# Kernel optimization log

Measured on AMD Instinct MI355X. Metric: run time of the kernel, lower is better.

The kernel has to match this reference:

```python
import jax, jax.numpy as jnp
import numpy as np

N_NODES = 100000
N_EDGES = 1000000
N_GRAPHS = 64
IN_F, H_F, N_CLS = 64, 64, 16
N_RELS = 8
N_BASES = 8  # DGL default: num_bases = num_rels when None


def setup_inputs() -> dict:
    key = jax.random.key(0)
    ks = jax.random.split(key, 16)
    in_feat = jax.random.normal(ks[0], (N_NODES, IN_F), dtype=jnp.float32)
    src = jax.random.randint(ks[1], (N_EDGES,), 0, N_NODES)
    dst = jax.random.randint(ks[2], (N_EDGES,), 0, N_NODES)
    etypes = jax.random.randint(ks[3], (N_EDGES,), 0, N_RELS)
    graph_ids = jnp.sort(jax.random.randint(ks[4], (N_NODES,), 0, N_GRAPHS))
    s1 = 1.0 / np.sqrt(IN_F)
    s2 = 1.0 / np.sqrt(H_F)
    bases1 = jax.random.normal(ks[5], (N_BASES, IN_F, H_F), dtype=jnp.float32) * s1
    coeff1 = jax.random.normal(ks[6], (N_RELS, N_BASES), dtype=jnp.float32) * (1.0 / np.sqrt(N_BASES))
    wself1 = jax.random.normal(ks[7], (IN_F, H_F), dtype=jnp.float32) * s1
    bias1 = jnp.zeros((H_F,), dtype=jnp.float32)
    bases2 = jax.random.normal(ks[8], (N_BASES, H_F, N_CLS), dtype=jnp.float32) * s2
    coeff2 = jax.random.normal(ks[9], (N_RELS, N_BASES), dtype=jnp.float32) * (1.0 / np.sqrt(N_BASES))
    wself2 = jax.random.normal(ks[10], (H_F, N_CLS), dtype=jnp.float32) * s2
    bias2 = jnp.zeros((N_CLS,), dtype=jnp.float32)
    return {"in_feat": in_feat, "src": src, "dst": dst, "etypes": etypes,
            "graph_ids": graph_ids, "bases1": bases1, "coeff1": coeff1,
            "wself1": wself1, "bias1": bias1, "bases2": bases2,
            "coeff2": coeff2, "wself2": wself2, "bias2": bias2}


def _rel_graph_conv(x, src, dst, etypes, bases, coeff, wself, bias):
    # Basis decomposition: W_r = sum_b coeff[r,b] * bases[b]
    W = jnp.einsum('rb,bio->rio', coeff, bases)          # [R, in, out]
    # Project every node under every relation (R small), then gather per edge.
    xw = jnp.einsum('ni,rio->rno', x, W)                 # [R, N, out]
    msg = xw[etypes, src]                                 # [E, out]
    agg = jax.ops.segment_sum(msg, dst, num_segments=x.shape[0])
    # DGL defaults: self_loop=True, bias=True
    return agg + x @ wself + bias


def reference(in_feat, src, dst, etypes, graph_ids,
              bases1, coeff1, wself1, bias1,
              bases2, coeff2, wself2, bias2):
    h = _rel_graph_conv(in_feat, src, dst, etypes, bases1, coeff1, wself1, bias1)
    h = jax.nn.relu(h)
    h = _rel_graph_conv(h, src, dst, etypes, bases2, coeff2, wself2, bias2)
    h = jax.nn.relu(h)
    # dgl.mean_nodes: per-graph mean over node features
    sums = jax.ops.segment_sum(h, graph_ids, num_segments=N_GRAPHS)   # [G, C]
    counts = jax.ops.segment_sum(jnp.ones((h.shape[0],), h.dtype), graph_ids,
                                 num_segments=N_GRAPHS)
    return sums / jnp.maximum(counts, 1.0)[:, None]
```

## Files before the change

### kernel.cpp

```cpp
#include <hip/hip_runtime.h>


typedef __attribute__((ext_vector_type(8))) short bf16x8;
typedef __attribute__((ext_vector_type(4))) float f32x4;

#define NBLK 256

__device__ __forceinline__ unsigned short f2bf(float f) {
    unsigned u = __float_as_uint(f);
    unsigned r = u + 0x7FFFu + ((u >> 16) & 1u);
    return (unsigned short)(r >> 16);
}

__device__ __forceinline__ float bf2f(unsigned short u) {
    return __uint_as_float(((unsigned)u) << 16);
}

__device__ __forceinline__ unsigned pk2(float lo, float hi) {
    unsigned r;
    asm("v_cvt_pk_bf16_f32 %0, %1, %2" : "=v"(r) : "v"(lo), "v"(hi));
    return r;
}

union cv16 { uint4 u; bf16x8 b; };

__device__ __forceinline__ void acc8(uint4 m, float* a) {
    a[0] += bf2f((unsigned short)m.x); a[1] += bf2f((unsigned short)(m.x >> 16));
    a[2] += bf2f((unsigned short)m.y); a[3] += bf2f((unsigned short)(m.y >> 16));
    a[4] += bf2f((unsigned short)m.z); a[5] += bf2f((unsigned short)(m.z >> 16));
    a[6] += bf2f((unsigned short)m.w); a[7] += bf2f((unsigned short)(m.w >> 16));
}

__global__ __launch_bounds__(256) void k_bhist_w(
    const int* __restrict__ dst, int* __restrict__ bh, int nE, int nBins,
    const float* __restrict__ bases1, const float* __restrict__ coeff1,
    const float* __restrict__ bases2, const float* __restrict__ coeff2,
    const float* __restrict__ wself1, const float* __restrict__ wself2,
    unsigned short* __restrict__ W1f, unsigned short* __restrict__ W2f,
    unsigned short* __restrict__ W1sf, unsigned short* __restrict__ W2sf) {
    if (blockIdx.x >= NBLK) {
        int r = blockIdx.x - NBLK;
        int tid = threadIdx.x;
        float c1[8], c2[8];
#pragma unroll
        for (int b = 0; b < 8; ++b) { c1[b] = coeff1[r * 8 + b]; c2[b] = coeff2[r * 8 + b]; }
        for (int idx = tid; idx < 4096; idx += 256) {
            int j = idx & 7, lane = (idx >> 3) & 63, nt = (idx >> 9) & 3, kt = idx >> 11;
            int i = kt * 32 + ((lane >> 4) << 3) + j;
            int jo = nt * 16 + (lane & 15);
            float s = 0.f;
#pragma unroll
            for (int b = 0; b < 8; ++b) s = fmaf(c1[b], bases1[b * 4096 + i * 64 + jo], s);
            W1f[r * 4096 + idx] = f2bf(s);
            if (r == 0) W1sf[idx] = f2bf(wself1[i * 64 + jo]);
        }
        for (int idx = tid; idx < 1024; idx += 256) {
            int j = idx & 7, lane = (idx >> 3) & 63, kt = idx >> 9;
            int i = kt * 32 + ((lane >> 4) << 3) + j;
            int jo = lane & 15;
            float s = 0.f;
#pragma unroll
            for (int b = 0; b < 8; ++b) s = fmaf(c2[b], bases2[b * 1024 + i * 16 + jo], s);
            W2f[r * 1024 + idx] = f2bf(s);
            if (r == 0) W2sf[idx] = f2bf(wself2[i * 16 + jo]);
        }
        return;
    }
    __shared__ int h[512];
    for (int i = threadIdx.x; i < 512; i += 256) h[i] = 0;
    __syncthreads();
    int blk = blockIdx.x;
    int ech = (nE + NBLK - 1) / NBLK;
    int e0 = blk * ech, e1 = min(e0 + ech, nE);
    for (int e = e0 + threadIdx.x; e < e1; e += 256)
        atomicAdd(&h[dst[e] >> 8], 1);
    __syncthreads();
    for (int t = threadIdx.x; t < nBins; t += 256) bh[t * NBLK + blk] = h[t];
}

__global__ __launch_bounds__(256) void k_scanblk(
    const int* __restrict__ in, int* __restrict__ outx,
    int* __restrict__ btot, int n) {
    __shared__ int sm[256];
    int tid = threadIdx.x;
    int i = blockIdx.x * 256 + tid;
    int d = (i < n) ? in[i] : 0;
    sm[tid] = d;
    __syncthreads();
#pragma unroll
    for (int off = 1; off < 256; off <<= 1) {
        int v = (tid >= off) ? sm[tid - off] : 0;
        __syncthreads();
        sm[tid] += v;
        __syncthreads();
    }
    if (i < n) outx[i] = sm[tid] - d;
    if (tid == 255) btot[blockIdx.x] = sm[255];
}

__global__ void k_scantop(const int* __restrict__ btot, int* __restrict__ boff, int nB) {
    __shared__ int sm[512];
    int t = threadIdx.x;
    int d = (t < nB) ? btot[t] : 0;
    sm[t] = d;
    __syncthreads();
#pragma unroll
    for (int off = 1; off < 512; off <<= 1) {
        int v = (t >= off) ? sm[t - off] : 0;
        __syncthreads();
        sm[t] += v;
        __syncthreads();
    }
    if (t < nB) boff[t] = sm[t] - d;
}

#define XW1S 44
__global__ __launch_bounds__(256) void k_mega(
    const int* __restrict__ dst, const int* __restrict__ src,
    const int* __restrict__ et, const int* __restrict__ bhs,
    const int* __restrict__ boff, int* __restrict__ payload,
    int nE, int nBins,
    const float* __restrict__ x,
    const unsigned short* __restrict__ W1f,
    const unsigned short* __restrict__ W1sf,
    const float* __restrict__ bias1,
    unsigned short* __restrict__ xw1, int nNodes) {
    __shared__ int cur[512];
    __shared__ unsigned lds[4][16 * XW1S];
    if (blockIdx.x < NBLK) {
        int blk = blockIdx.x;
        for (int t = threadIdx.x; t < nBins; t += 256)
            cur[t] = bhs[t * NBLK + blk] + boff[t];
        __syncthreads();
        int ech = (nE + NBLK - 1) / NBLK;
        int e0 = blk * ech, e1 = min(e0 + ech, nE);
        for (int e = e0 + threadIdx.x; e < e1; e += 256) {
            int d = dst[e];
            int pos = atomicAdd(&cur[d >> 8], 1);
            payload[pos] = ((src[e] * 9 + et[e]) << 8) | (d & 255);
        }
        return;
    }
    int lane = threadIdx.x & 63;
    int wid = (int)(threadIdx.x >> 6);
    int tile = (blockIdx.x - NBLK) * 4 + wid;
    int n0 = tile * 16;
    if (n0 >= nNodes) return;
    int sA = n0 + (lane & 15);
    if (sA >= nNodes) sA = nNodes - 1;
    const float* xrow = x + (size_t)sA * 64 + ((lane >> 4) << 3);
    bf16x8 a[2];
#pragma unroll
    for (int kt = 0; kt < 2; ++kt) {
        f32x4 u0 = *(const f32x4*)(xrow + kt * 32);
        f32x4 u1 = *(const f32x4*)(xrow + kt * 32 + 4);
        cv16 c;
        c.u.x = pk2(u0[0], u0[1]);
        c.u.y = pk2(u0[2], u0[3]);
        c.u.z = pk2(u1[0], u1[1]);
        c.u.w = pk2(u1[2], u1[3]);
        a[kt] = c.b;
    }
    float bj[4];
#pragma unroll
    for (int nt = 0; nt < 4; ++nt) bj[nt] = bias1[nt * 16 + (lane & 15)];
    unsigned* L = lds[wid];
    const int even = !(lane & 1);
    const int cpair = (lane & 14) >> 1;
    int row2 = lane >> 2, ch = lane & 3;
    int nOut = n0 + row2;
    for (int r = 0; r < 9; ++r) {
        const unsigned short* Wf = (r < 8) ? (W1f + r * 4096) : W1sf;
        f32x4 z = {0.f, 0.f, 0.f, 0.f};
        f32x4 acc[4] = {z, z, z, z};
#pragma unroll
        for (int kt = 0; kt < 2; ++kt)
#pragma unroll
            for (int nt = 0; nt < 4; ++nt) {
                bf16x8 b = *(const bf16x8*)(Wf + (kt * 4 + nt) * 512 + lane * 8);
                acc[nt] = __builtin_amdgcn_mfma_f32_16x16x32_bf16(a[kt], b, acc[nt], 0, 0, 0);
            }
        if (r == 8) {
#pragma unroll
            for (int nt = 0; nt < 4; ++nt)
#pragma unroll
                for (int reg = 0; reg < 4; ++reg) acc[nt][reg] += bj[nt];
        }
#pragma unroll
        for (int reg = 0; reg < 4; ++reg) {
            int row = ((lane >> 4) << 2) + reg;
#pragma unroll
            for (int nt = 0; nt < 4; ++nt) {
                float mine = acc[nt][reg];
                float oth = __shfl_xor(mine, 1, 64);
                unsigned pk = even ? pk2(mine, oth) : pk2(oth, mine);
                if (even ? (nt < 2) : (nt >= 2)) L[row * XW1S + cpair + nt * 8] = pk;
            }
        }
        if (nOut < nNodes) {
            uint4 v0 = *(uint4*)&L[row2 * XW1S + ch * 4];
            uint4 v1 = *(uint4*)&L[row2 * XW1S + 16 + ch * 4];
            uint4* mp = (uint4*)(xw1 + ((size_t)nOut * 9 + r) * 64);
            mp[ch] = v0;
            mp[4 + ch] = v1;
        }
    }
}

__global__ __launch_bounds__(256) void k_brefine(
    const int* __restrict__ payload, const int* __restrict__ bhs,
    const int* __restrict__ boff,
    int* __restrict__ skey, int* __restrict__ nodeoff,
    int nE, int nBins, int nNodes) {
    __shared__ int h[256];
    __shared__ int cur[256];
    __shared__ int sm[256];
    int b = blockIdx.x;
    int e0 = bhs[b * NBLK] + boff[b];
    int e1 = (b + 1 < nBins) ? (bhs[(b + 1) * NBLK] + boff[b + 1]) : nE;
    int t = threadIdx.x;
    h[t] = 0;
    __syncthreads();
    for (int e = e0 + t; e < e1; e += 256)
        atomicAdd(&h[payload[e] & 255], 1);
    __syncthreads();
    int d = h[t];
    sm[t] = d;
    __syncthreads();
#pragma unroll
    for (int off = 1; off < 256; off <<= 1) {
        int v = (t >= off) ? sm[t - off] : 0;
        __syncthreads();
        sm[t] += v;
        __syncthreads();
    }
    int excl = sm[t] - d;
    cur[t] = excl;
    int n = (b << 8) + t;
    if (n < nNodes) nodeoff[n] = e0 + excl;
    __syncthreads();
    for (int e = e0 + t; e < e1; e += 256) {
        int pay = payload[e];
        int pos = atomicAdd(&cur[pay & 255], 1);
        skey[e0 + pos] = pay >> 8;
    }
    if (b == 0 && t == 0) nodeoff[nNodes] = nE;
}

__global__ __launch_bounds__(256) void k_f1(
    const unsigned short* __restrict__ xw1, const int* __restrict__ skey,
    const int* __restrict__ nodeoff,
    const unsigned short* __restrict__ W2f,
    const unsigned short* __restrict__ W2sf,
    const float* __restrict__ bias2,
    unsigned short* __restrict__ xw2, int nNodes) {
    __shared__ uint4 hbuf[64][9];
    __shared__ unsigned tlds[4][16 * 12];
    int t = threadIdx.x;
    int n0blk = blockIdx.x * 64;
    int gl = t & 7;
    int grp = t >> 3;
    for (int pass = 0; pass < 2; ++pass) {
        int nn = pass * 32 + grp;
        int n = n0blk + nn;
        uint4 p = {0, 0, 0, 0};
        if (n < nNodes) {
            int s0 = nodeoff[n], s1 = nodeoff[n + 1];
            uint4 v = *(const uint4*)(xw1 + ((size_t)n * 9 + 8) * 64 + gl * 8);
            float a[8];
            a[0] = bf2f((unsigned short)v.x); a[1] = bf2f((unsigned short)(v.x >> 16));
            a[2] = bf2f((unsigned short)v.y); a[3] = bf2f((unsigned short)(v.y >> 16));
            a[4] = bf2f((unsigned short)v.z); a[5] = bf2f((unsigned short)(v.z >> 16));
            a[6] = bf2f((unsigned short)v.w); a[7] = bf2f((unsigned short)(v.w >> 16));
            int i = s0;
            for (; i + 4 <= s1; i += 4) {
                int k0 = skey[i], k1 = skey[i + 1], k2 = skey[i + 2], k3 = skey[i + 3];
                uint4 m0 = *(const uint4*)(xw1 + (size_t)k0 * 64 + gl * 8);
                uint4 m1 = *(const uint4*)(xw1 + (size_t)k1 * 64 + gl * 8);
                uint4 m2 = *(const uint4*)(xw1 + (size_t)k2 * 64 + gl * 8);
                uint4 m3 = *(const uint4*)(xw1 + (size_t)k3 * 64 + gl * 8);
                acc8(m0, a); acc8(m1, a); acc8(m2, a); acc8(m3, a);
            }
            for (; i < s1; ++i) {
                uint4 m = *(const uint4*)(xw1 + (size_t)skey[i] * 64 + gl * 8);
                acc8(m, a);
            }
#pragma unroll
            for (int q = 0; q < 8; ++q) a[q] = fmaxf(a[q], 0.f);
            p.x = pk2(a[0], a[1]);
            p.y = pk2(a[2], a[3]);
            p.z = pk2(a[4], a[5]);
            p.w = pk2(a[6], a[7]);
        }
        hbuf[nn][gl] = p;
    }
    __syncthreads();
    int lane = t & 63;
    int w = t >> 6;
    int arow = w * 16 + (lane & 15);
    cv16 c0, c1;
    c0.u = hbuf[arow][lane >> 4];
    c1.u = hbuf[arow][4 + (lane >> 4)];
    bf16x8 a0 = c0.b, a1 = c1.b;
    float bj = bias2[lane & 15];
    unsigned* L = tlds[w];
    const int even = !(lane & 1);
    const int cpair = (lane & 14) >> 1;
    int row2 = lane >> 1, ch = lane & 1;
    int nOut = n0blk + w * 16 + row2;
    for (int r = 0; r < 9; ++r) {
        const unsigned short* Wf = (r < 8) ? (W2f + r * 1024) : W2sf;
        bf16x8 b0 = *(const bf16x8*)(Wf + lane * 8);
        bf16x8 b1 = *(const bf16x8*)(Wf + 512 + lane * 8);
        f32x4 acc = {0.f, 0.f, 0.f, 0.f};
        acc = __builtin_amdgcn_mfma_f32_16x16x32_bf16(a0, b0, acc, 0, 0, 0);
        acc = __builtin_amdgcn_mfma_f32_16x16x32_bf16(a1, b1, acc, 0, 0, 0);
        if (r == 8) {
#pragma unroll
            for (int reg = 0; reg < 4; ++reg) acc[reg] += bj;
        }
#pragma unroll
        for (int reg = 0; reg < 4; ++reg) {
            int row = ((lane >> 4) << 2) + reg;
            float mine = acc[reg];
            float oth = __shfl_xor(mine, 1, 64);
            unsigned pk = even ? pk2(mine, oth) : pk2(oth, mine);
            if (even ? (reg < 2) : (reg >= 2)) L[row * 12 + cpair] = pk;
        }
        if (lane < 32 && nOut < nNodes) {
            uint4 v = *(uint4*)&L[row2 * 12 + ch * 4];
            ((uint4*)(xw2 + ((size_t)nOut * 9 + r) * 16))[ch] = v;
        }
    }
}

__global__ __launch_bounds__(256) void k_seg2f(
    unsigned short* __restrict__ xw2, const int* __restrict__ skey,
    const int* __restrict__ nodeoff, int nNodes) {
    int gl = threadIdx.x & 1;
    int grp = (int)((blockIdx.x * blockDim.x + threadIdx.x) >> 1);
    int nG = (int)((gridDim.x * blockDim.x) >> 1);
    for (int n = grp; n < nNodes; n += nG) {
        int s0 = nodeoff[n], s1 = nodeoff[n + 1];
        uint4 v = *(const uint4*)(xw2 + ((size_t)n * 9 + 8) * 16 + gl * 8);
        float a[8];
        a[0] = bf2f((unsigned short)v.x); a[1] = bf2f((unsigned short)(v.x >> 16));
        a[2] = bf2f((unsigned short)v.y); a[3] = bf2f((unsigned short)(v.y >> 16));
        a[4] = bf2f((unsigned short)v.z); a[5] = bf2f((unsigned short)(v.z >> 16));
        a[6] = bf2f((unsigned short)v.w); a[7] = bf2f((unsigned short)(v.w >> 16));
        int i = s0;
        for (; i + 4 <= s1; i += 4) {
            int k0 = skey[i], k1 = skey[i + 1], k2 = skey[i + 2], k3 = skey[i + 3];
            uint4 m0 = *(const uint4*)(xw2 + (size_t)k0 * 16 + gl * 8);
            uint4 m1 = *(const uint4*)(xw2 + (size_t)k1 * 16 + gl * 8);
            uint4 m2 = *(const uint4*)(xw2 + (size_t)k2 * 16 + gl * 8);
            uint4 m3 = *(const uint4*)(xw2 + (size_t)k3 * 16 + gl * 8);
            acc8(m0, a); acc8(m1, a); acc8(m2, a); acc8(m3, a);
        }
        for (; i < s1; ++i) {
            uint4 m = *(const uint4*)(xw2 + (size_t)skey[i] * 16 + gl * 8);
            acc8(m, a);
        }
        uint4 p;
        p.x = pk2(a[0], a[1]);
        p.y = pk2(a[2], a[3]);
        p.z = pk2(a[4], a[5]);
        p.w = pk2(a[6], a[7]);
        *(uint4*)(xw2 + ((size_t)n * 9 + 8) * 16 + gl * 8) = p;
    }
}

__global__ __launch_bounds__(256) void k_pool(
    const unsigned short* __restrict__ xw2, const int* __restrict__ gid,
    float* __restrict__ out, int nNodes) {
    __shared__ float sm[256];
    __shared__ int bnd[2];
    int g = blockIdx.x;
    int t = threadIdx.x;
    if (t < 2) {
        int target = g + t;
        int lo = 0, hi = nNodes;
        while (lo < hi) {
            int mid = (lo + hi) >> 1;
            if (gid[mid] < target) lo = mid + 1; else hi = mid;
        }
        bnd[t] = lo;
    }
    __syncthreads();
    int s0 = bnd[0], s1 = bnd[1];
    int c = t & 15, idx = t >> 4;
    float acc = 0.f;
    for (int n = s0 + idx; n < s1; n += 16)
        acc += fmaxf(bf2f(xw2[((size_t)n * 9 + 8) * 16 + c]), 0.f);
    sm[t] = acc;
    __syncthreads();
#pragma unroll
    for (int off = 128; off >= 16; off >>= 1) {
        if (t < off) sm[t] += sm[t + off];
        __syncthreads();
    }
    if (t < 16) {
        float cnt = (float)(s1 - s0);
        out[g * 16 + t] = sm[t] / fmaxf(cnt, 1.f);
    }
}

extern "C" void kernel_launch(void* const* d_in, const int* in_sizes, int n_in,
                              void* d_out, int out_size, void* d_ws, size_t ws_size,
                              hipStream_t stream) {
    const float* x      = (const float*)d_in[0];
    const int*   src    = (const int*)d_in[1];
    const int*   dst    = (const int*)d_in[2];
    const int*   et     = (const int*)d_in[3];
    const int*   gid    = (const int*)d_in[4];
    const float* bases1 = (const float*)d_in[5];
    const float* coeff1 = (const float*)d_in[6];
    const float* wself1 = (const float*)d_in[7];
    const float* bias1  = (const float*)d_in[8];
    const float* bases2 = (const float*)d_in[9];
    const float* coeff2 = (const float*)d_in[10];
    const float* wself2 = (const float*)d_in[11];
    const float* bias2  = (const float*)d_in[12];
    float* out = (float*)d_out;

    int nNodes = in_sizes[0] / 64;
    int nE = in_sizes[1];
    int nBins = (nNodes + 255) >> 8;
    int nBh = nBins * NBLK;

    char* ws = (char*)d_ws;
    unsigned short* W1f  = (unsigned short*)(ws);
    unsigned short* W2f  = (unsigned short*)(ws + 65536);
    unsigned short* W1sf = (unsigned short*)(ws + 81920);
    unsigned short* W2sf = (unsigned short*)(ws + 90112);
    int*   payload = (int*)(ws + 92160);
    int*   skey    = (int*)(ws + 4092160);
    int*   nodeoff = (int*)(ws + 8092160);
    int*   bh      = (int*)(ws + 8492288);
    int*   bhs     = (int*)(ws + 8892672);
    int*   btot    = (int*)(ws + 9293056);
    int*   boff    = (int*)(ws + 9295104);
    unsigned short* xw1 = (unsigned short*)(ws + 9297152);
    unsigned short* xw2 = (unsigned short*)(ws + 124497152);

    int tiles = (nNodes + 15) / 16;
    int xwb = (tiles + 3) / 4;
    int f1b = (nNodes + 63) / 64;
    int scb = (nBh + 255) / 256;

    hipLaunchKernelGGL(k_bhist_w, dim3(NBLK + 8), dim3(256), 0, stream,
                       dst, bh, nE, nBins,
                       bases1, coeff1, bases2, coeff2, wself1, wself2,
                       W1f, W2f, W1sf, W2sf);
    hipLaunchKernelGGL(k_scanblk, dim3(scb), dim3(256), 0, stream,
                       bh, bhs, btot, nBh);
    hipLaunchKernelGGL(k_scantop, dim3(1), dim3(512), 0, stream, btot, boff, scb);
    hipLaunchKernelGGL(k_mega, dim3(NBLK + xwb), dim3(256), 0, stream,
                       dst, src, et, bhs, boff, payload, nE, nBins,
                       x, W1f, W1sf, bias1, xw1, nNodes);
    hipLaunchKernelGGL(k_brefine, dim3(nBins), dim3(256), 0, stream,
                       payload, bhs, boff, skey, nodeoff, nE, nBins, nNodes);
    hipLaunchKernelGGL(k_f1, dim3(f1b), dim3(256), 0, stream,
                       xw1, skey, nodeoff, W2f, W2sf, bias2, xw2, nNodes);
    hipLaunchKernelGGL(k_seg2f, dim3(1024), dim3(256), 0, stream,
                       xw2, skey, nodeoff, nNodes);
    hipLaunchKernelGGL(k_pool, dim3(64), dim3(256), 0, stream,
                       xw2, gid, out, nNodes);
}
```

Baseline: 167.4 us.

## Split layer-1 projection across scatter and refine kernels to overlap work

The layer-1 node projection (xw1 MFMA tiles) was previously fused only with the edge scatter kernel, and the bucket-refine kernel ran alone with just nBins blocks. Now a single kernel template handles both phases, and each launch computes half of the projection tiles, so the refine phase also has independent GEMM work to fill the GPU. The aim is to hide the low-occupancy refine kernel behind useful compute. In exchange the LDS footprint per block grows and the block-index roles are reordered, with projection blocks first and sort blocks last.

```diff
diff --git a/kernel.cpp b/kernel.cpp
--- a/kernel.cpp
+++ b/kernel.cpp
@@ -5,6 +5,7 @@
 typedef __attribute__((ext_vector_type(4))) float f32x4;
 
 #define NBLK 256
+#define XW1S 44
 
 __device__ __forceinline__ unsigned short f2bf(float f) {
     unsigned u = __float_as_uint(f);
@@ -114,36 +115,71 @@
     if (t < nB) boff[t] = sm[t] - d;
 }
 
-#define XW1S 44
-__global__ __launch_bounds__(256) void k_mega(
+__global__ __launch_bounds__(256) void k_megax(
+    int phase, int tileOff, int xwbThis,
     const int* __restrict__ dst, const int* __restrict__ src,
     const int* __restrict__ et, const int* __restrict__ bhs,
     const int* __restrict__ boff, int* __restrict__ payload,
-    int nE, int nBins,
+    int* __restrict__ skey, int* __restrict__ nodeoff, int nE, int nBins,
     const float* __restrict__ x,
     const unsigned short* __restrict__ W1f,
     const unsigned short* __restrict__ W1sf,
     const float* __restrict__ bias1,
     unsigned short* __restrict__ xw1, int nNodes) {
-    __shared__ int cur[512];
     __shared__ unsigned lds[4][16 * XW1S];
-    if (blockIdx.x < NBLK) {
-        int blk = blockIdx.x;
-        for (int t = threadIdx.x; t < nBins; t += 256)
-            cur[t] = bhs[t * NBLK + blk] + boff[t];
-        __syncthreads();
-        int ech = (nE + NBLK - 1) / NBLK;
-        int e0 = blk * ech, e1 = min(e0 + ech, nE);
-        for (int e = e0 + threadIdx.x; e < e1; e += 256) {
-            int d = dst[e];
-            int pos = atomicAdd(&cur[d >> 8], 1);
-            payload[pos] = ((src[e] * 9 + et[e]) << 8) | (d & 255);
+    __shared__ int scur[512];
+    __shared__ int sh[256];
+    __shared__ int ssm[256];
+    if ((int)blockIdx.x >= xwbThis) {
+        int sb = blockIdx.x - xwbThis;
+        int t = threadIdx.x;
+        if (phase == 0) {
+            for (int q = t; q < nBins; q += 256)
+                scur[q] = bhs[q * NBLK + sb] + boff[q];
+            __syncthreads();
+            int ech = (nE + NBLK - 1) / NBLK;
+            int e0 = sb * ech, e1 = min(e0 + ech, nE);
+            for (int e = e0 + t; e < e1; e += 256) {
+                int d = dst[e];
+                int pos = atomicAdd(&scur[d >> 8], 1);
+                payload[pos] = ((src[e] * 9 + et[e]) << 8) | (d & 255);
+            }
+        } else {
+            int b = sb;
+            int e0 = bhs[b * NBLK] + boff[b];
+            int e1 = (b + 1 < nBins) ? (bhs[(b + 1) * NBLK] + boff[b + 1]) : nE;
+            sh[t] = 0;
+            __syncthreads();
+            for (int e = e0 + t; e < e1; e += 256)
+                atomicAdd(&sh[payload[e] & 255], 1);
+            __syncthreads();
+            int d = sh[t];
+            ssm[t] = d;
+            __syncthreads();
+#pragma unroll
+            for (int off = 1; off < 256; off <<= 1) {
+                int v = (t >= off) ? ssm[t - off] : 0;
+                __syncthreads();
+                ssm[t] += v;
+                __syncthreads();
+            }
+            int excl = ssm[t] - d;
+            scur[t] = excl;
+            int n = (b << 8) + t;
+            if (n < nNodes) nodeoff[n] = e0 + excl;
+            __syncthreads();
+            for (int e = e0 + t; e < e1; e += 256) {
+                int pay = payload[e];
+                int pos = atomicAdd(&scur[pay & 255], 1);
+                skey[e0 + pos] = pay >> 8;
+            }
+            if (b == 0 && t == 0) nodeoff[nNodes] = nE;
         }
         return;
     }
     int lane = threadIdx.x & 63;
     int wid = (int)(threadIdx.x >> 6);
-    int tile = (blockIdx.x - NBLK) * 4 + wid;
+    int tile = tileOff + blockIdx.x * 4 + wid;
     int n0 = tile * 16;
     if (n0 >= nNodes) return;
     int sA = n0 + (lane & 15);
@@ -205,46 +241,6 @@
             mp[4 + ch] = v1;
         }
     }
-}
-
-__global__ __launch_bounds__(256) void k_brefine(
-    const int* __restrict__ payload, const int* __restrict__ bhs,
-    const int* __restrict__ boff,
-    int* __restrict__ skey, int* __restrict__ nodeoff,
-    int nE, int nBins, int nNodes) {
-    __shared__ int h[256];
-    __shared__ int cur[256];
-    __shared__ int sm[256];
-    int b = blockIdx.x;
-    int e0 = bhs[b * NBLK] + boff[b];
-    int e1 = (b + 1 < nBins) ? (bhs[(b + 1) * NBLK] + boff[b + 1]) : nE;
-    int t = threadIdx.x;
-    h[t] = 0;
-    __syncthreads();
-    for (int e = e0 + t; e < e1; e += 256)
-        atomicAdd(&h[payload[e] & 255], 1);
-    __syncthreads();
-    int d = h[t];
-    sm[t] = d;
-    __syncthreads();
-#pragma unroll
-    for (int off = 1; off < 256; off <<= 1) {
-        int v = (t >= off) ? sm[t - off] : 0;
-        __syncthreads();
-        sm[t] += v;
-        __syncthreads();
-    }
-    int excl = sm[t] - d;
-    cur[t] = excl;
-    int n = (b << 8) + t;
-    if (n < nNodes) nodeoff[n] = e0 + excl;
-    __syncthreads();
-    for (int e = e0 + t; e < e1; e += 256) {
-        int pay = payload[e];
-        int pos = atomicAdd(&cur[pay & 255], 1);
-        skey[e0 + pos] = pay >> 8;
-    }
-    if (b == 0 && t == 0) nodeoff[nNodes] = nE;
 }
 
 __global__ __launch_bounds__(256) void k_f1(
@@ -444,7 +440,10 @@
     unsigned short* xw2 = (unsigned short*)(ws + 124497152);
 
     int tiles = (nNodes + 15) / 16;
-    int xwb = (tiles + 3) / 4;
+    int tA = ((tiles / 2) + 3) & ~3;
+    int xwbA = tA / 4;
+    int tB = tiles - tA;
+    int xwbB = (tB + 3) / 4;
     int f1b = (nNodes + 63) / 64;
     int scb = (nBh + 255) / 256;
 
@@ -455,11 +454,14 @@
     hipLaunchKernelGGL(k_scanblk, dim3(scb), dim3(256), 0, stream,
                        bh, bhs, btot, nBh);
     hipLaunchKernelGGL(k_scantop, dim3(1), dim3(512), 0, stream, btot, boff, scb);
-    hipLaunchKernelGGL(k_mega, dim3(NBLK + xwb), dim3(256), 0, stream,
-                       dst, src, et, bhs, boff, payload, nE, nBins,
+    hipLaunchKernelGGL(k_megax, dim3(xwbA + NBLK), dim3(256), 0, stream,
+                       0, 0, xwbA,
+                       dst, src, et, bhs, boff, payload, skey, nodeoff, nE, nBins,
                        x, W1f, W1sf, bias1, xw1, nNodes);
-    hipLaunchKernelGGL(k_brefine, dim3(nBins), dim3(256), 0, stream,
-                       payload, bhs, boff, skey, nodeoff, nE, nBins, nNodes);
+    hipLaunchKernelGGL(k_megax, dim3(xwbB + nBins), dim3(256), 0, stream,
+                       1, tA, xwbB,
+                       dst, src, et, bhs, boff, payload, skey, nodeoff, nE, nBins,
+                       x, W1f, W1sf, bias1, xw1, nNodes);
     hipLaunchKernelGGL(k_f1, dim3(f1b), dim3(256), 0, stream,
                        xw1, skey, nodeoff, W2f, W2sf, bias2, xw2, nNodes);
     hipLaunchKernelGGL(k_seg2f, dim3(1024), dim3(256), 0, stream,
```

After: 171.2 us. 1.02x slower.
